# Kernel optimization log

Measured on AMD Instinct MI355X. Metric: run time of the kernel, lower is better.

## Reference

```python
import jax, jax.numpy as jnp
import numpy as np

TLAMBDA = 0.5
DELTA = 0.1
PROP_LAYERS = 2
LN_EPS = 1e-12
MASK_NEG = -10000.0
N_HEADS = 4


def _ln(x, g, b):
    m = x.mean(-1, keepdims=True)
    v = ((x - m) ** 2).mean(-1, keepdims=True)
    return (x - m) * jax.lax.rsqrt(v + LN_EPS) * g + b


def _l2norm(x):
    # F.normalize(p=2, dim=-1) with eps=1e-12
    n = jnp.sqrt((x * x).sum(-1, keepdims=True))
    return x / jnp.maximum(n, 1e-12)


def _sparse_prop(op):
    # op: [B, N, 2] rows of (col_idx, weight). result[b,j,m] = w_j*w_m if idx_j==idx_m else 0
    idx = op[..., 0].astype(jnp.int32)
    w = op[..., 1]
    eq = idx[:, :, None] == idx[:, None, :]
    return jnp.where(eq, w[:, :, None] * w[:, None, :], jnp.zeros((), op.dtype))


def _prop(t, P):
    enc = t
    for _ in range(PROP_LAYERS):
        t = jnp.einsum('bnm,bme->bne', P, t) + DELTA * enc
    return t


def _bert_layer(h, mask, Wq, bq, Wk, bk, Wv, bv, Wo, bo, g1, b1, Wi, bi, Wf, bf, g2, b2):
    AN, S, E = h.shape
    dh = E // N_HEADS

    def heads(x):
        return x.reshape(AN, S, N_HEADS, dh).transpose(0, 2, 1, 3)

    q = heads(h @ Wq + bq)
    k = heads(h @ Wk + bk)
    v = heads(h @ Wv + bv)
    scores = jnp.einsum('ahsd,ahtd->ahst', q, k) / np.float32(np.sqrt(dh)) + mask
    probs = jax.nn.softmax(scores, axis=-1)
    ctx = jnp.einsum('ahst,ahtd->ahsd', probs, v).transpose(0, 2, 1, 3).reshape(AN, S, E)
    a = _ln(ctx @ Wo + bo + h, g1, b1)
    f = jax.nn.gelu(a @ Wi + bi, approximate=False)
    return _ln(f @ Wf + bf + a, g2, b2)


def reference(token_edges_batch, hidden_states, attention_mask, query_embedding, key_embedding,
              user_operator, item_operator, distance_embedding, centrality_embedding,
              Wq, bq, Wk, bk, Wv, bv, Wo, bo, ln_att_g, ln_att_b, Wi, bi, Wf, bf, ln_ffn_g, ln_ffn_b,
              W_agg, b_agg, W_d1, b_d1, ln1_g, ln1_b, W_d2, b_d2, ln2_g, ln2_b):
    B, N, _ = token_edges_batch.shape
    AN, S, E = hidden_states.shape
    L = Wq.shape[0]

    U = _sparse_prop(user_operator)   # [B, N, N]
    I = _sparse_prop(item_operator)
    sub_next_q = jnp.zeros((B, N, E), hidden_states.dtype)
    sub_next_k = jnp.zeros((B, N, E), hidden_states.dtype)
    mask0 = attention_mask.at[..., :4].set(MASK_NEG)

    hs = hidden_states.reshape(B, N, S, E)
    all_hs = []
    for i in range(L):
        all_hs.append(hs)
        if i > 0:
            hs = (hs.at[:, :, 0].set(query_embedding)
                    .at[:, :, 1].set(key_embedding)
                    .at[:, :, 2].set(distance_embedding)
                    .at[:, :, 3].set(centrality_embedding))
        p1 = _ln(_prop(TLAMBDA * query_embedding + sub_next_q, U) @ W_d1 + b_d1, ln1_g, ln1_b)
        p2 = _ln(_prop(TLAMBDA * key_embedding + sub_next_k, I) @ W_d2 + b_d2, ln2_g, ln2_b)
        mask = mask0 if i == 0 else attention_mask
        h = _bert_layer(hs.reshape(AN, S, E), mask,
                        Wq[i], bq[i], Wk[i], bk[i], Wv[i], bv[i], Wo[i], bo[i],
                        ln_att_g[i], ln_att_b[i], Wi[i], bi[i], Wf[i], bf[i], ln_ffn_g[i], ln_ffn_b[i])
        hs = h.reshape(B, N, S, E)
        sub_next_q = hs[:, :, 0, :]
        sub_next_k = hs[:, :, 1, :]
        snt = _l2norm(hs[:, 0, 4, :])                       # [B, E]
        p = jnp.concatenate([snt, p1[:, 0, :], p2[:, 1, :]], axis=1)  # [B, 3E]
        agg = _l2norm(jax.nn.relu(p @ W_agg[i] + b_agg[i]))
        hs = hs.at[:, 0, 4, :].set(agg)
    all_hs.append(hs)

    out1 = all_hs[L - 1][:, 0, 4:, :].mean(axis=1)
    out2 = all_hs[L][:, 0, 4:, :].mean(axis=1)
    return 0.5 * (out1 + out2)


def setup_inputs() -> dict:
    key = jax.random.key(0)
    ks = jax.random.split(key, 40)
    B, N, S, E, L, FF = 64, 64, 32, 256, 2, 1024
    AN = B * N
    f = jnp.float32
    inp = {}
    inp['token_edges_batch'] = jax.random.randint(ks[0], (B, N, 8), 0, 100)
    inp['hidden_states'] = jax.random.normal(ks[1], (AN, S, E), f)
    inp['attention_mask'] = jnp.zeros((AN, 1, 1, S), f)
    inp['query_embedding'] = jax.random.normal(ks[2], (B, N, E), f)
    inp['key_embedding'] = jax.random.normal(ks[3], (B, N, E), f)
    inp['distance_embedding'] = jax.random.normal(ks[4], (B, N, E), f)
    inp['centrality_embedding'] = jax.random.normal(ks[5], (B, N, E), f)

    def make_op(k1, k2):
        idx = jax.random.randint(k1, (B, N), 0, 16).astype(f)
        w = jax.random.uniform(k2, (B, N), f)
        return jnp.stack([idx, w], axis=-1)

    inp['user_operator'] = make_op(ks[6], ks[7])
    inp['item_operator'] = make_op(ks[8], ks[9])

    sc = 0.02
    def w(k, shape):
        return jax.random.normal(k, shape, f) * sc

    inp['Wq'] = w(ks[10], (L, E, E)); inp['bq'] = jnp.zeros((L, E), f)
    inp['Wk'] = w(ks[11], (L, E, E)); inp['bk'] = jnp.zeros((L, E), f)
    inp['Wv'] = w(ks[12], (L, E, E)); inp['bv'] = jnp.zeros((L, E), f)
    inp['Wo'] = w(ks[13], (L, E, E)); inp['bo'] = jnp.zeros((L, E), f)
    inp['ln_att_g'] = jnp.ones((L, E), f); inp['ln_att_b'] = jnp.zeros((L, E), f)
    inp['Wi'] = w(ks[14], (L, E, FF)); inp['bi'] = jnp.zeros((L, FF), f)
    inp['Wf'] = w(ks[15], (L, FF, E)); inp['bf'] = jnp.zeros((L, E), f)
    inp['ln_ffn_g'] = jnp.ones((L, E), f); inp['ln_ffn_b'] = jnp.zeros((L, E), f)
    inp['W_agg'] = w(ks[16], (L, 3 * E, E)); inp['b_agg'] = jnp.zeros((L, E), f)
    inp['W_d1'] = w(ks[17], (E, E)); inp['b_d1'] = jnp.zeros((E,), f)
    inp['ln1_g'] = jnp.ones((E,), f); inp['ln1_b'] = jnp.zeros((E,), f)
    inp['W_d2'] = w(ks[18], (E, E)); inp['b_d2'] = jnp.zeros((E,), f)
    inp['ln2_g'] = jnp.ones((E,), f); inp['ln2_b'] = jnp.zeros((E,), f)
    return inp
```

## Files before the change

kernel.cpp:

```cpp
#include <hip/hip_runtime.h>
#include <math.h>

#define E 256
#define SEQ 32
#define FF 1024
#define NEG_MASK -10000.0f

typedef __attribute__((ext_vector_type(8))) short bf16x8;
typedef __attribute__((ext_vector_type(4))) short s16x4;
typedef __attribute__((ext_vector_type(4))) float f32x4;
typedef __attribute__((ext_vector_type(16))) float f32x16;

__device__ __forceinline__ float bf2f(unsigned short u) {
  unsigned v = ((unsigned)u) << 16; float f; __builtin_memcpy(&f, &v, 4); return f;
}
__device__ __forceinline__ unsigned short f2bf(float f) {
  unsigned u; __builtin_memcpy(&u, &f, 4);
  unsigned r = (u + 0x7fffu + ((u >> 16) & 1u)) >> 16;
  return (unsigned short)r;
}
__device__ __forceinline__ s16x4 f2bf4(float4 v) {
  s16x4 r;
  r[0] = (short)f2bf(v.x); r[1] = (short)f2bf(v.y);
  r[2] = (short)f2bf(v.z); r[3] = (short)f2bf(v.w);
  return r;
}
__device__ __forceinline__ f32x4 mfma16(bf16x8 a, bf16x8 b, f32x4 c) {
  return __builtin_amdgcn_mfma_f32_16x16x32_bf16(a, b, c, 0, 0, 0);
}
__device__ __forceinline__ f32x16 mfma32(bf16x8 a, bf16x8 b, f32x16 c) {
  return __builtin_amdgcn_mfma_f32_32x32x16_bf16(a, b, c, 0, 0, 0);
}
__device__ __forceinline__ float block_sum256(float v, float* tmp4) {
  #pragma unroll
  for (int o = 32; o > 0; o >>= 1) v += __shfl_down(v, o);
  int wid = threadIdx.x >> 6, lane = threadIdx.x & 63;
  if (lane == 0) tmp4[wid] = v;
  __syncthreads();
  float r = tmp4[0] + tmp4[1] + tmp4[2] + tmp4[3];
  __syncthreads();
  return r;
}

__global__ __launch_bounds__(256) void wprep_kernel(
    const float* __restrict__ Wq, const float* __restrict__ Wk,
    const float* __restrict__ Wv, const float* __restrict__ Wo,
    const float* __restrict__ Wi, const float* __restrict__ Wf,
    unsigned short* wqt, unsigned short* wkt, unsigned short* wvt,
    unsigned short* wot, unsigned short* wit, unsigned short* wft) {
  int type = blockIdx.y, ll = blockIdx.z, t = threadIdx.x;
  const float* src; unsigned short* dst; int Kd, Nd, m32;
  switch (type) {
    case 0: src = Wq + (size_t)ll * 65536;  dst = wqt + (size_t)ll * 65536;  Kd = 256;  Nd = 256;  m32 = 0; break;
    case 1: src = Wk + (size_t)ll * 65536;  dst = wkt + (size_t)ll * 65536;  Kd = 256;  Nd = 256;  m32 = 0; break;
    case 2: src = Wv + (size_t)ll * 65536;  dst = wvt + (size_t)ll * 65536;  Kd = 256;  Nd = 256;  m32 = 0; break;
    case 3: src = Wo + (size_t)ll * 65536;  dst = wot + (size_t)ll * 65536;  Kd = 256;  Nd = 256;  m32 = 0; break;
    case 4: src = Wi + (size_t)ll * 262144; dst = wit + (size_t)ll * 262144; Kd = 256;  Nd = 1024; m32 = 1; break;
    default: src = Wf + (size_t)ll * 262144; dst = wft + (size_t)ll * 262144; Kd = 1024; Nd = 256; m32 = 1; break;
  }
  int frag = blockIdx.x * 4 + (t >> 6);
  int l = t & 63;
  int nkc = m32 ? (Kd >> 4) : (Kd >> 5);
  int nfrag = (m32 ? (Nd >> 5) : (Nd >> 4)) * nkc;
  if (frag >= nfrag) return;
  int n, k0;
  if (m32) { n = (frag / nkc) * 32 + (l & 31); k0 = (frag % nkc) * 16 + (l >> 5) * 8; }
  else     { n = (frag / nkc) * 16 + (l & 15); k0 = (frag % nkc) * 32 + (l >> 4) * 8; }
  unsigned short vv[8];
  #pragma unroll
  for (int j = 0; j < 8; ++j) vv[j] = f2bf(src[(size_t)(k0 + j) * Nd + n]);
  unsigned short* o = dst + (size_t)frag * 512 + l * 8;
  #pragma unroll
  for (int j = 0; j < 8; ++j) o[j] = vv[j];
}

__global__ __launch_bounds__(256) void prop_ln_kernel(
    const float* __restrict__ emb_q, const float* __restrict__ emb_k,
    const float* snq,
    const float* __restrict__ uop, const float* __restrict__ iop,
    const float* __restrict__ Wd1, const float* __restrict__ bd1,
    const float* __restrict__ g1v, const float* __restrict__ b1v,
    const float* __restrict__ Wd2, const float* __restrict__ bd2,
    const float* __restrict__ g2v, const float* __restrict__ b2v,
    float* __restrict__ out1, float* __restrict__ out2) {
  int sel = blockIdx.y;
  const float* emb = sel ? emb_k : emb_q;
  const float* op  = sel ? iop : uop;
  const float* Wd  = sel ? Wd2 : Wd1;
  const float* bd  = sel ? bd2 : bd1;
  const float* g   = sel ? g2v : g1v;
  const float* bvec= sel ? b2v : b1v;
  float* outp      = sel ? out2 : out1;
  int row = sel;
  __shared__ float t0s[64][E];
  __shared__ float s1[16 * E];
  __shared__ float s2[16 * E];
  __shared__ float wv[64];
  __shared__ int gi[64];
  __shared__ float t2row[E];
  __shared__ float tmp4[4];
  int b = blockIdx.x, e = threadIdx.x;
  if (e < 64) {
    wv[e] = op[(b * 64 + e) * 2 + 1];
    gi[e] = (int)op[(b * 64 + e) * 2 + 0];
  }
  for (int gg = 0; gg < 16; ++gg) { s1[gg * E + e] = 0.f; s2[gg * E + e] = 0.f; }
  for (int n = 0; n < 64; ++n) {
    float t0 = 0.5f * emb[(size_t)(b * 64 + n) * E + e];
    if (snq) t0 += snq[((size_t)(b * 64 + n) * 2 + sel) * E + e];
    t0s[n][e] = t0;
  }
  __syncthreads();
  for (int n = 0; n < 64; ++n) s1[gi[n] * E + e] += wv[n] * t0s[n][e];
  for (int n = 0; n < 64; ++n) {
    float t1 = wv[n] * s1[gi[n] * E + e] + 0.1f * t0s[n][e];
    s2[gi[n] * E + e] += wv[n] * t1;
  }
  float t2 = wv[row] * s2[gi[row] * E + e] + 0.1f * t0s[row][e];
  t2row[e] = t2;
  __syncthreads();
  float y = bd[e];
  for (int k = 0; k < E; ++k) y = fmaf(t2row[k], Wd[k * E + e], y);
  float ssum = block_sum256(y, tmp4);
  float qsum = block_sum256(y * y, tmp4);
  float m = ssum * (1.f / E);
  float var = qsum * (1.f / E) - m * m;
  outp[b * E + e] = (y - m) * rsqrtf(var + 1e-12f) * g[e] + bvec[e];
}

__global__ __launch_bounds__(256, 4) void seq_attn_mfma(
    const float* __restrict__ hidden,
    const unsigned short* __restrict__ wqt, const float* __restrict__ bq,
    const unsigned short* __restrict__ wkt, const float* __restrict__ bk,
    const unsigned short* __restrict__ wvt, const float* __restrict__ bv,
    const float* __restrict__ mask, unsigned short* __restrict__ ctx_all,
    unsigned short* __restrict__ Kf, unsigned short* __restrict__ Vf) {
  __shared__ __align__(16) unsigned short aT[32][264];
  __shared__ __align__(16) unsigned short kvb[32][272];
  __shared__ __align__(16) unsigned short qs16[2][264];
  __shared__ float pr[4][2][36];
  int a = blockIdx.x, t = threadIdx.x;
  int w = t >> 6, l = t & 63;
  int lm = l & 15, lkq = l >> 4, lk = lkq << 3;
  size_t hb = (size_t)a * (SEQ * E);
  #pragma unroll
  for (int i = 0; i < 8; ++i) {
    int p = i * 256 + t; int row = p >> 6, c4 = (p & 63) << 2;
    float4 v = *(const float4*)&hidden[hb + row * E + c4];
    *(s16x4*)&aT[row][c4] = f2bf4(v);
  }
  __syncthreads();
  bool isn0 = ((a & 63) == 0);
  int nb = a >> 6;
  f32x4 zz = {0.f, 0.f, 0.f, 0.f};
  #pragma unroll
  for (int nt = 0; nt < 4; ++nt) {
    int ncol = w * 64 + nt * 16 + lm;
    const unsigned short* bkrow = wkt + ((size_t)(w * 4 + nt) * 8) * 512 + l * 8;
    const unsigned short* bqrow = wqt + ((size_t)(w * 4 + nt) * 8) * 512 + l * 8;
    bf16x8 bk8[8], bq8[8];
    #pragma unroll
    for (int kc = 0; kc < 8; ++kc) bk8[kc] = *(const bf16x8*)(bkrow + kc * 512);
    #pragma unroll
    for (int kc = 0; kc < 8; ++kc) bq8[kc] = *(const bf16x8*)(bqrow + kc * 512);
    f32x4 ak0 = zz, ak1 = zz, aq = zz;
    #pragma unroll
    for (int kc = 0; kc < 8; ++kc) {
      bf16x8 a0 = *(const bf16x8*)&aT[lm][kc * 32 + lk];
      bf16x8 a1 = *(const bf16x8*)&aT[16 + lm][kc * 32 + lk];
      ak0 = mfma16(a0, bk8[kc], ak0);
      ak1 = mfma16(a1, bk8[kc], ak1);
      aq  = mfma16(a0, bq8[kc], aq);
    }
    float bb = bk[ncol];
    #pragma unroll
    for (int r = 0; r < 4; ++r) {
      int rw = (lkq << 2) + r;
      float v0 = ak0[r] + bb, v1 = ak1[r] + bb;
      kvb[rw][ncol] = f2bf(v0);
      kvb[16 + rw][ncol] = f2bf(v1);
      if (isn0) {
        Kf[((size_t)nb * 32 + rw) * 256 + ncol] = f2bf(v0);
        Kf[((size_t)nb * 32 + 16 + rw) * 256 + ncol] = f2bf(v1);
      }
    }
    if (lkq == 0) {
      float bqv = bq[ncol];
      qs16[0][ncol] = f2bf(aq[0] + bqv);
      qs16[1][ncol] = f2bf(aq[1] + bqv);
    }
  }
  __syncthreads();
  {
    f32x4 sc0 = zz, sc1 = zz;
    #pragma unroll
    for (int kc2 = 0; kc2 < 2; ++kc2) {
      bf16x8 aq = *(const bf16x8*)&qs16[lm & 1][w * 64 + kc2 * 32 + lk];
      bf16x8 b0 = *(const bf16x8*)&kvb[lm][w * 64 + kc2 * 32 + lk];
      bf16x8 b1 = *(const bf16x8*)&kvb[16 + lm][w * 64 + kc2 * 32 + lk];
      sc0 = mfma16(aq, b0, sc0);
      sc1 = mfma16(aq, b1, sc1);
    }
    float mv0 = (lm < 4) ? NEG_MASK : mask[(size_t)a * SEQ + lm];
    float mv1 = mask[(size_t)a * SEQ + 16 + lm];
    #pragma unroll
    for (int r = 0; r < 2; ++r) {
      float s0 = sc0[r] * 0.125f + mv0;
      float s1 = sc1[r] * 0.125f + mv1;
      float mx = fmaxf(s0, s1);
      mx = fmaxf(mx, __shfl_xor(mx, 1));
      mx = fmaxf(mx, __shfl_xor(mx, 2));
      mx = fmaxf(mx, __shfl_xor(mx, 4));
      mx = fmaxf(mx, __shfl_xor(mx, 8));
      float e0 = expf(s0 - mx), e1 = expf(s1 - mx);
      float se = e0 + e1;
      se += __shfl_xor(se, 1); se += __shfl_xor(se, 2);
      se += __shfl_xor(se, 4); se += __shfl_xor(se, 8);
      float inv = 1.f / se;
      if (lkq == 0) {
        pr[w][r][lm] = e0 * inv;
        pr[w][r][16 + lm] = e1 * inv;
      }
    }
  }
  __syncthreads();
  #pragma unroll
  for (int nt = 0; nt < 4; ++nt) {
    int ncol = w * 64 + nt * 16 + lm;
    const unsigned short* bvrow = wvt + ((size_t)(w * 4 + nt) * 8) * 512 + l * 8;
    bf16x8 bv8[8];
    #pragma unroll
    for (int kc = 0; kc < 8; ++kc) bv8[kc] = *(const bf16x8*)(bvrow + kc * 512);
    f32x4 av0 = zz, av1 = zz;
    #pragma unroll
    for (int kc = 0; kc < 8; ++kc) {
      bf16x8 a0 = *(const bf16x8*)&aT[lm][kc * 32 + lk];
      bf16x8 a1 = *(const bf16x8*)&aT[16 + lm][kc * 32 + lk];
      av0 = mfma16(a0, bv8[kc], av0);
      av1 = mfma16(a1, bv8[kc], av1);
    }
    float bb = bv[ncol];
    #pragma unroll
    for (int r = 0; r < 4; ++r) {
      int rw = (lkq << 2) + r;
      float v0 = av0[r] + bb, v1 = av1[r] + bb;
      kvb[rw][ncol] = f2bf(v0);
      kvb[16 + rw][ncol] = f2bf(v1);
      if (isn0) {
        Vf[((size_t)nb * 32 + rw) * 256 + ncol] = f2bf(v0);
        Vf[((size_t)nb * 32 + 16 + rw) * 256 + ncol] = f2bf(v1);
      }
    }
  }
  __syncthreads();
  {
    float o0 = 0.f, o1 = 0.f;
    #pragma unroll
    for (int tt = 0; tt < 32; ++tt) {
      float vv = bf2f(kvb[tt][t]);
      o0 = fmaf(pr[w][0][tt], vv, o0);
      o1 = fmaf(pr[w][1][tt], vv, o1);
    }
    ctx_all[((size_t)a * 2 + 0) * E + t] = f2bf(o0);
    ctx_all[((size_t)a * 2 + 1) * E + t] = f2bf(o1);
  }
}

__global__ __launch_bounds__(256) void gemm_bias_kernel(
    const float* __restrict__ Af, const unsigned short* __restrict__ Bt,
    const float* __restrict__ bias, unsigned short* __restrict__ outb) {
  __shared__ __align__(16) unsigned short aT[32][264];
  int t = threadIdx.x, w = t >> 6, l = t & 63;
  int lm = l & 15, lkq = l >> 4, lk = lkq << 3;
  int row0 = blockIdx.x * 32;
  #pragma unroll
  for (int i = 0; i < 8; ++i) {
    int p = i * 256 + t; int row = p >> 6, c4 = (p & 63) << 2;
    int gr = row0 + row;
    int src = ((gr >> 5) << 11) + (gr & 31);
    float4 v = *(const float4*)&Af[(size_t)src * E + c4];
    *(s16x4*)&aT[row][c4] = f2bf4(v);
  }
  __syncthreads();
  f32x4 zz = {0.f, 0.f, 0.f, 0.f};
  #pragma unroll
  for (int nt = 0; nt < 4; ++nt) {
    int ncol = w * 64 + nt * 16 + lm;
    const unsigned short* brow = Bt + ((size_t)(w * 4 + nt) * 8) * 512 + l * 8;
    bf16x8 b8[8];
    #pragma unroll
    for (int kc = 0; kc < 8; ++kc) b8[kc] = *(const bf16x8*)(brow + kc * 512);
    f32x4 c0 = zz, c1 = zz;
    #pragma unroll
    for (int kc = 0; kc < 8; ++kc) {
      bf16x8 a0 = *(const bf16x8*)&aT[lm][kc * 32 + lk];
      bf16x8 a1 = *(const bf16x8*)&aT[16 + lm][kc * 32 + lk];
      c0 = mfma16(a0, b8[kc], c0);
      c1 = mfma16(a1, b8[kc], c1);
    }
    float bb = bias[ncol];
    #pragma unroll
    for (int r = 0; r < 4; ++r) {
      int rw = (lkq << 2) + r;
      outb[(size_t)(row0 + rw) * E + ncol] = f2bf(c0[r] + bb);
      outb[(size_t)(row0 + 16 + rw) * E + ncol] = f2bf(c1[r] + bb);
    }
  }
}

__global__ __launch_bounds__(256) void qkv1_kernel(
    const unsigned short* __restrict__ Ab,
    const unsigned short* __restrict__ wq, const float* __restrict__ bqv,
    const unsigned short* __restrict__ wk, const float* __restrict__ bkv,
    const unsigned short* __restrict__ wv, const float* __restrict__ bvv,
    unsigned short* q2, unsigned short* k2, unsigned short* v2) {
  __shared__ __align__(16) unsigned short aT[32][264];
  int t = threadIdx.x, w = t >> 6, l = t & 63;
  int lm = l & 15, lkq = l >> 4, lk = lkq << 3;
  int row0 = blockIdx.x * 32;
  int m = blockIdx.y;
  const unsigned short* Wt = (m == 0) ? wq : (m == 1) ? wk : wv;
  const float* bb = (m == 0) ? bqv : (m == 1) ? bkv : bvv;
  unsigned short* outb = (m == 0) ? q2 : (m == 1) ? k2 : v2;
  #pragma unroll
  for (int i = 0; i < 4; ++i) {
    int p = i * 256 + t; int row = p >> 5, c8 = (p & 31) << 3;
    *(s16x4*)&aT[row][c8] = *(const s16x4*)&Ab[(size_t)(row0 + row) * E + c8];
    *(s16x4*)&aT[row][c8 + 4] = *(const s16x4*)&Ab[(size_t)(row0 + row) * E + c8 + 4];
  }
  __syncthreads();
  f32x4 zz = {0.f, 0.f, 0.f, 0.f};
  #pragma unroll
  for (int nt = 0; nt < 4; ++nt) {
    int ncol = w * 64 + nt * 16 + lm;
    const unsigned short* brow = Wt + ((size_t)(w * 4 + nt) * 8) * 512 + l * 8;
    bf16x8 b8[8];
    #pragma unroll
    for (int kc = 0; kc < 8; ++kc) b8[kc] = *(const bf16x8*)(brow + kc * 512);
    f32x4 c0 = zz, c1 = zz;
    #pragma unroll
    for (int kc = 0; kc < 8; ++kc) {
      bf16x8 a0 = *(const bf16x8*)&aT[lm][kc * 32 + lk];
      bf16x8 a1 = *(const bf16x8*)&aT[16 + lm][kc * 32 + lk];
      c0 = mfma16(a0, b8[kc], c0);
      c1 = mfma16(a1, b8[kc], c1);
    }
    float bv2 = bb[ncol];
    #pragma unroll
    for (int r = 0; r < 4; ++r) {
      int rw = (lkq << 2) + r;
      outb[(size_t)(row0 + rw) * E + ncol] = f2bf(c0[r] + bv2);
      outb[(size_t)(row0 + 16 + rw) * E + ncol] = f2bf(c1[r] + bv2);
    }
  }
}

__global__ __launch_bounds__(256) void attnf_kernel(
    const unsigned short* __restrict__ Q, const unsigned short* __restrict__ K,
    const unsigned short* __restrict__ V, unsigned short* __restrict__ CTX,
    const float* __restrict__ mask, int set4) {
  int b = blockIdx.x, h = blockIdx.y, t = threadIdx.x;
  __shared__ float qsh[32][65], ksh[32][65], vsh[32][65];
  __shared__ float pr[32][33];
  size_t base = (size_t)b * (SEQ * E) + h * 64;
  for (int i = 0; i < 8; ++i) {
    int p = i * 256 + t; int s = p >> 6, d = p & 63;
    qsh[s][d] = bf2f(Q[base + s * E + d]);
    ksh[s][d] = bf2f(K[base + s * E + d]);
    vsh[s][d] = bf2f(V[base + s * E + d]);
  }
  __syncthreads();
  for (int i = 0; i < 4; ++i) {
    int p = i * 256 + t; int s = p >> 5, tt = p & 31;
    float acc = 0.f;
    #pragma unroll
    for (int d = 0; d < 64; ++d) acc = fmaf(qsh[s][d], ksh[tt][d], acc);
    float mv = mask[(size_t)b * 2048 + tt];
    if (set4 && tt < 4) mv = NEG_MASK;
    pr[s][tt] = acc * 0.125f + mv;
  }
  __syncthreads();
  int rrow = t >> 3, l8 = t & 7;
  float vals[4];
  float mx = -1e30f;
  #pragma unroll
  for (int ii = 0; ii < 4; ++ii) { vals[ii] = pr[rrow][l8 + ii * 8]; mx = fmaxf(mx, vals[ii]); }
  mx = fmaxf(mx, __shfl_xor(mx, 1));
  mx = fmaxf(mx, __shfl_xor(mx, 2));
  mx = fmaxf(mx, __shfl_xor(mx, 4));
  float se = 0.f;
  #pragma unroll
  for (int ii = 0; ii < 4; ++ii) { vals[ii] = expf(vals[ii] - mx); se += vals[ii]; }
  se += __shfl_xor(se, 1); se += __shfl_xor(se, 2); se += __shfl_xor(se, 4);
  float inv = 1.f / se;
  #pragma unroll
  for (int ii = 0; ii < 4; ++ii) pr[rrow][l8 + ii * 8] = vals[ii] * inv;
  __syncthreads();
  for (int i = 0; i < 8; ++i) {
    int p = i * 256 + t; int s = p >> 6, d = p & 63;
    float acc = 0.f;
    #pragma unroll
    for (int tt = 0; tt < SEQ; ++tt) acc = fmaf(pr[s][tt], vsh[tt][d], acc);
    CTX[base + s * E + d] = f2bf(acc);
  }
}

__device__ __forceinline__ int map_res(int gr) {
  if (gr < 8192) return ((gr >> 1) << 5) + (gr & 1);
  int rr = gr - 8192;
  return ((rr >> 5) << 11) + (rr & 31);
}

__global__ __launch_bounds__(256) void tailA_mfma(
    const unsigned short* __restrict__ ctx,
    const unsigned short* __restrict__ wo, const float* __restrict__ bo,
    const float* __restrict__ Res, int resmode,
    const float* __restrict__ g1, const float* __restrict__ b1,
    unsigned short* __restrict__ a_bf, float* __restrict__ a_f32) {
  __shared__ __align__(16) unsigned short aT[32][264];
  __shared__ float sT[32][257];
  __shared__ float prs[32][4], prq[32][4];
  int t = threadIdx.x, w = t >> 6, l = t & 63;
  int row0 = blockIdx.x * 32;
  #pragma unroll
  for (int i = 0; i < 8; ++i) {
    int p = i * 256 + t; int row = p >> 6, c4 = (p & 63) << 2;
    *(s16x4*)&aT[row][c4] = *(const s16x4*)&ctx[(size_t)(row0 + row) * E + c4];
  }
  __syncthreads();
  {
    int lm = l & 15, lkq = l >> 4, lk = lkq << 3;
    f32x4 zz = {0.f, 0.f, 0.f, 0.f};
    #pragma unroll
    for (int nt = 0; nt < 4; ++nt) {
      int ncol = w * 64 + nt * 16 + lm;
      const unsigned short* brow = wo + ((size_t)(w * 4 + nt) * 8) * 512 + l * 8;
      bf16x8 b8[8];
      #pragma unroll
      for (int kc = 0; kc < 8; ++kc) b8[kc] = *(const bf16x8*)(brow + kc * 512);
      f32x4 c0 = zz, c1 = zz;
      #pragma unroll
      for (int kc = 0; kc < 8; ++kc) {
        bf16x8 a0 = *(const bf16x8*)&aT[lm][kc * 32 + lk];
        bf16x8 a1 = *(const bf16x8*)&aT[16 + lm][kc * 32 + lk];
        c0 = mfma16(a0, b8[kc], c0);
        c1 = mfma16(a1, b8[kc], c1);
      }
      float bb = bo[ncol];
      #pragma unroll
      for (int r = 0; r < 4; ++r) {
        int rw = (lkq << 2) + r;
        int rr0 = resmode ? map_res(row0 + rw) : (row0 + rw);
        int rr1 = resmode ? map_res(row0 + 16 + rw) : (row0 + 16 + rw);
        sT[rw][ncol] = c0[r] + bb + Res[(size_t)rr0 * E + ncol];
        sT[16 + rw][ncol] = c1[r] + bb + Res[(size_t)rr1 * E + ncol];
      }
    }
  }
  __syncthreads();
  {
    int wid = t >> 6, lane = t & 63;
    float vcache[32];
    for (int r = 0; r < 32; ++r) {
      float v = sT[r][t];
      vcache[r] = v;
      float s = v, q = v * v;
      #pragma unroll
      for (int o = 32; o > 0; o >>= 1) { s += __shfl_down(s, o); q += __shfl_down(q, o); }
      if (lane == 0) { prs[r][wid] = s; prq[r][wid] = q; }
    }
    __syncthreads();
    #pragma unroll
    for (int r = 0; r < 32; ++r) {
      float Sv = prs[r][0] + prs[r][1] + prs[r][2] + prs[r][3];
      float Qv = prq[r][0] + prq[r][1] + prq[r][2] + prq[r][3];
      float m = Sv * (1.f / E), var = Qv * (1.f / E) - m * m;
      float val = (vcache[r] - m) * rsqrtf(var + 1e-12f) * g1[t] + b1[t];
      a_f32[(size_t)(row0 + r) * E + t] = val;
      a_bf[(size_t)(row0 + r) * E + t] = f2bf(val);
    }
  }
}

__global__ __launch_bounds__(512) void ffnB_kernel(
    const unsigned short* __restrict__ a_bf,
    const unsigned short* __restrict__ wi, const float* __restrict__ bi,
    const unsigned short* __restrict__ wf,
    float* __restrict__ part, size_t pstride) {
  __shared__ __align__(16) unsigned short aT[32][264];
  __shared__ __align__(16) unsigned short fT[32][264];
  int t = threadIdx.x, w = t >> 6, l = t & 63;
  int lm = l & 31, lk = (l >> 5) << 3;
  int row0 = blockIdx.x * 32, qh = blockIdx.y;
  #pragma unroll
  for (int i = 0; i < 2; ++i) {
    int chunk = i * 512 + t; int row = chunk >> 5, c8 = (chunk & 31) << 3;
    *(s16x4*)&aT[row][c8] = *(const s16x4*)&a_bf[(size_t)(row0 + row) * E + c8];
    *(s16x4*)&aT[row][c8 + 4] = *(const s16x4*)&a_bf[(size_t)(row0 + row) * E + c8 + 4];
  }
  __syncthreads();
  f32x16 zz16 = {0};
  {
    const unsigned short* brow = wi + ((size_t)(qh * 8 + w) * 16) * 512 + l * 8;
    bf16x8 b16[16];
    #pragma unroll
    for (int kc = 0; kc < 16; ++kc) b16[kc] = *(const bf16x8*)(brow + kc * 512);
    f32x16 c = zz16;
    #pragma unroll
    for (int kc = 0; kc < 16; ++kc) {
      bf16x8 a = *(const bf16x8*)&aT[lm][kc * 16 + lk];
      c = mfma32(a, b16[kc], c);
    }
    int lcol = w * 32 + lm;
    float bib = bi[qh * 256 + lcol];
    #pragma unroll
    for (int reg = 0; reg < 16; ++reg) {
      int row = (reg & 3) + 8 * (reg >> 2) + 4 * (l >> 5);
      float x = c[reg] + bib;
      fT[row][lcol] = f2bf(0.5f * x * (1.f + erff(x * 0.70710678118654752f)));
    }
  }
  __syncthreads();
  {
    const unsigned short* brow = wf + ((size_t)(w * 64 + qh * 16)) * 512 + l * 8;
    bf16x8 b16[16];
    #pragma unroll
    for (int kc = 0; kc < 16; ++kc) b16[kc] = *(const bf16x8*)(brow + kc * 512);
    f32x16 c = zz16;
    #pragma unroll
    for (int kc = 0; kc < 16; ++kc) {
      bf16x8 a = *(const bf16x8*)&fT[lm][kc * 16 + lk];
      c = mfma32(a, b16[kc], c);
    }
    float* po = part + (size_t)qh * pstride;
    int col = w * 32 + lm;
    #pragma unroll
    for (int reg = 0; reg < 16; ++reg) {
      int row = (reg & 3) + 8 * (reg >> 2) + 4 * (l >> 5);
      po[(size_t)(row0 + row) * E + col] = c[reg];
    }
  }
}

__global__ __launch_bounds__(256) void ffnC_kernel(
    const float* __restrict__ part, size_t pstride,
    const float* __restrict__ bfv, const float* __restrict__ a_f32,
    const float* __restrict__ g2, const float* __restrict__ b2,
    float* __restrict__ out0, float* __restrict__ out1, int split) {
  __shared__ float prs[32][4], prq[32][4];
  int t = threadIdx.x;
  int row0 = blockIdx.x * 32;
  int wid = t >> 6, lane = t & 63;
  float bb = bfv[t];
  float vcache[32];
  for (int r = 0; r < 32; ++r) {
    size_t idx = (size_t)(row0 + r) * E + t;
    float v = part[idx] + part[pstride + idx] + part[2 * pstride + idx] +
              part[3 * pstride + idx] + bb + a_f32[idx];
    vcache[r] = v;
    float s = v, q = v * v;
    #pragma unroll
    for (int o = 32; o > 0; o >>= 1) { s += __shfl_down(s, o); q += __shfl_down(q, o); }
    if (lane == 0) { prs[r][wid] = s; prq[r][wid] = q; }
  }
  __syncthreads();
  #pragma unroll
  for (int r = 0; r < 32; ++r) {
    float Sv = prs[r][0] + prs[r][1] + prs[r][2] + prs[r][3];
    float Qv = prq[r][0] + prq[r][1] + prq[r][2] + prq[r][3];
    float m = Sv * (1.f / E), var = Qv * (1.f / E) - m * m;
    float val = (vcache[r] - m) * rsqrtf(var + 1e-12f) * g2[t] + b2[t];
    int gr = row0 + r;
    if (gr < split) out0[(size_t)gr * E + t] = val;
    else            out1[(size_t)(gr - split) * E + t] = val;
  }
}

__global__ __launch_bounds__(256) void agg_build_kernel(
    const float* __restrict__ h1n0,
    const float* __restrict__ p1, const float* __restrict__ p2,
    const float* __restrict__ Wagg, const float* __restrict__ bagg,
    const float* __restrict__ qe, const float* __restrict__ ke,
    const float* __restrict__ de, const float* __restrict__ ce,
    float* __restrict__ agg0,
    float* __restrict__ h2f, unsigned short* __restrict__ h2b) {
  __shared__ float pv[768];
  __shared__ float tmp4[4];
  int b = blockIdx.x, t = threadIdx.x;
  float x = h1n0[(size_t)b * (SEQ * E) + 4 * E + t];
  float n2 = block_sum256(x * x, tmp4);
  pv[t] = x / fmaxf(sqrtf(n2), 1e-12f);
  pv[256 + t] = p1[b * E + t];
  pv[512 + t] = p2[b * E + t];
  __syncthreads();
  float y = bagg[t];
  for (int u = 0; u < 768; ++u) y = fmaf(pv[u], Wagg[u * E + t], y);
  y = fmaxf(y, 0.f);
  float n3 = block_sum256(y * y, tmp4);
  float aggv = y / fmaxf(sqrtf(n3), 1e-12f);
  agg0[b * E + t] = aggv;
  size_t eb = (size_t)(b * 64) * E + t;
  size_t ob = (size_t)b * (SEQ * E);
  float v;
  v = qe[eb];  h2f[ob + 0 * E + t] = v; h2b[ob + 0 * E + t] = f2bf(v);
  v = ke[eb];  h2f[ob + 1 * E + t] = v; h2b[ob + 1 * E + t] = f2bf(v);
  v = de[eb];  h2f[ob + 2 * E + t] = v; h2b[ob + 2 * E + t] = f2bf(v);
  v = ce[eb];  h2f[ob + 3 * E + t] = v; h2b[ob + 3 * E + t] = f2bf(v);
  h2f[ob + 4 * E + t] = aggv; h2b[ob + 4 * E + t] = f2bf(aggv);
  for (int s = 5; s < SEQ; ++s) {
    v = h1n0[ob + s * E + t];
    h2f[ob + s * E + t] = v; h2b[ob + s * E + t] = f2bf(v);
  }
}

__global__ __launch_bounds__(256) void agg_kernel(
    const float* __restrict__ hbase,
    const float* __restrict__ p1, const float* __restrict__ p2,
    const float* __restrict__ Wagg, const float* __restrict__ bagg,
    float* __restrict__ outp) {
  __shared__ float pv[768];
  __shared__ float tmp4[4];
  int b = blockIdx.x, t = threadIdx.x;
  float x = hbase[(size_t)b * (SEQ * E) + 4 * E + t];
  float n2 = block_sum256(x * x, tmp4);
  pv[t] = x / fmaxf(sqrtf(n2), 1e-12f);
  pv[256 + t] = p1[b * E + t];
  pv[512 + t] = p2[b * E + t];
  __syncthreads();
  float y = bagg[t];
  for (int u = 0; u < 768; ++u) y = fmaf(pv[u], Wagg[u * E + t], y);
  y = fmaxf(y, 0.f);
  float n3 = block_sum256(y * y, tmp4);
  outp[b * E + t] = y / fmaxf(sqrtf(n3), 1e-12f);
}

__global__ __launch_bounds__(256) void out_kernel(
    const float* __restrict__ h1n0, const float* __restrict__ agg0,
    const float* __restrict__ h2, const float* __restrict__ agg1,
    float* __restrict__ outp) {
  int b = blockIdx.x, t = threadIdx.x;
  size_t ob = (size_t)b * (SEQ * E);
  float s1v = agg0[b * E + t];
  float s2v = agg1[b * E + t];
  for (int s = 5; s < SEQ; ++s) { s1v += h1n0[ob + s * E + t]; s2v += h2[ob + s * E + t]; }
  outp[b * E + t] = 0.5f * (s1v + s2v) * (1.f / 28.f);
}

extern "C" void kernel_launch(void* const* d_in, const int* in_sizes, int n_in,
                              void* d_out, int out_size, void* d_ws, size_t ws_size,
                              hipStream_t stream) {
  (void)in_sizes; (void)n_in; (void)out_size;
  const float* hidden = (const float*)d_in[1];
  const float* amask  = (const float*)d_in[2];
  const float* qemb   = (const float*)d_in[3];
  const float* kemb   = (const float*)d_in[4];
  const float* demb   = (const float*)d_in[5];
  const float* cemb   = (const float*)d_in[6];
  const float* uop    = (const float*)d_in[7];
  const float* iop    = (const float*)d_in[8];
  const float* Wq = (const float*)d_in[9];  const float* bq = (const float*)d_in[10];
  const float* Wk = (const float*)d_in[11]; const float* bk = (const float*)d_in[12];
  const float* Wv = (const float*)d_in[13]; const float* bv = (const float*)d_in[14];
  const float* Wo = (const float*)d_in[15]; const float* bo = (const float*)d_in[16];
  const float* g1 = (const float*)d_in[17]; const float* b1 = (const float*)d_in[18];
  const float* Wi = (const float*)d_in[19]; const float* bi = (const float*)d_in[20];
  const float* Wf = (const float*)d_in[21]; const float* bf = (const float*)d_in[22];
  const float* g2 = (const float*)d_in[23]; const float* b2 = (const float*)d_in[24];
  const float* Wagg = (const float*)d_in[25]; const float* bagg = (const float*)d_in[26];
  const float* Wd1 = (const float*)d_in[27]; const float* bd1 = (const float*)d_in[28];
  const float* l1g = (const float*)d_in[29]; const float* l1b = (const float*)d_in[30];
  const float* Wd2 = (const float*)d_in[31]; const float* bd2 = (const float*)d_in[32];
  const float* l2g = (const float*)d_in[33]; const float* l2b = (const float*)d_in[34];

  char* cur = (char*)d_ws;
  auto alloc_us = [&](size_t n) { unsigned short* p = (unsigned short*)cur; cur += ((n * 2 + 255) & ~(size_t)255); return p; };
  auto alloc_f  = [&](size_t n) { float* p = (float*)cur; cur += ((n * 4 + 255) & ~(size_t)255); return p; };
  unsigned short* wqt = alloc_us(131072);
  unsigned short* wkt = alloc_us(131072);
  unsigned short* wvt = alloc_us(131072);
  unsigned short* wot = alloc_us(131072);
  unsigned short* wit = alloc_us(524288);
  unsigned short* wft = alloc_us(524288);
  unsigned short* ctx_all = alloc_us((size_t)10240 * 256);
  unsigned short* qn0 = alloc_us((size_t)2048 * 256);
  unsigned short* Kf  = alloc_us((size_t)2048 * 256);
  unsigned short* Vf  = alloc_us((size_t)2048 * 256);
  unsigned short* h2inb = alloc_us((size_t)2048 * 256);
  unsigned short* a_bf = alloc_us((size_t)10240 * 256);
  unsigned short* q2b = alloc_us((size_t)2048 * 256);
  unsigned short* k2b = alloc_us((size_t)2048 * 256);
  unsigned short* v2b = alloc_us((size_t)2048 * 256);
  unsigned short* ctx1 = alloc_us((size_t)2048 * 256);
  float* a_f32 = alloc_f((size_t)10240 * 256);
  float* part  = alloc_f((size_t)4 * 10240 * 256);
  float* h101  = alloc_f((size_t)4096 * 2 * 256);
  float* h1n0  = alloc_f((size_t)2048 * 256);
  float* h2inf = alloc_f((size_t)2048 * 256);
  float* h2    = alloc_f((size_t)2048 * 256);
  float* p1_0  = alloc_f(64 * 256);
  float* p2_0  = alloc_f(64 * 256);
  float* p1_1  = alloc_f(64 * 256);
  float* p2_1  = alloc_f(64 * 256);
  float* agg0  = alloc_f(64 * 256);
  float* agg1  = alloc_f(64 * 256);
  if ((size_t)(cur - (char*)d_ws) > ws_size) return;
  const size_t PSTRIDE = (size_t)10240 * 256;

  wprep_kernel<<<dim3(128, 6, 2), 256, 0, stream>>>(Wq, Wk, Wv, Wo, Wi, Wf,
                                                    wqt, wkt, wvt, wot, wit, wft);

  prop_ln_kernel<<<dim3(64, 2), 256, 0, stream>>>(qemb, kemb, nullptr, uop, iop,
                                                  Wd1, bd1, l1g, l1b, Wd2, bd2, l2g, l2b,
                                                  p1_0, p2_0);
  seq_attn_mfma<<<4096, 256, 0, stream>>>(hidden, wqt, bq, wkt, bk, wvt, bv,
                                          amask, ctx_all, Kf, Vf);
  gemm_bias_kernel<<<64, 256, 0, stream>>>(hidden, wqt, bq, qn0);
  attnf_kernel<<<dim3(64, 4), 256, 0, stream>>>(qn0, Kf, Vf, ctx_all + (size_t)8192 * 256,
                                                amask, 1);
  tailA_mfma<<<320, 256, 0, stream>>>(ctx_all, wot, bo, hidden, 1, g1, b1, a_bf, a_f32);
  ffnB_kernel<<<dim3(320, 4), 512, 0, stream>>>(a_bf, wit, bi, wft, part, PSTRIDE);
  ffnC_kernel<<<320, 256, 0, stream>>>(part, PSTRIDE, bf, a_f32, g2, b2,
                                       h101, h1n0, 8192);
  agg_build_kernel<<<64, 256, 0, stream>>>(h1n0, p1_0, p2_0, Wagg, bagg,
                                           qemb, kemb, demb, cemb, agg0, h2inf, h2inb);

  prop_ln_kernel<<<dim3(64, 2), 256, 0, stream>>>(qemb, kemb, h101, uop, iop,
                                                  Wd1, bd1, l1g, l1b, Wd2, bd2, l2g, l2b,
                                                  p1_1, p2_1);
  qkv1_kernel<<<dim3(64, 3), 256, 0, stream>>>(h2inb,
                                               wqt + 65536, bq + E,
                                               wkt + 65536, bk + E,
                                               wvt + 65536, bv + E,
                                               q2b, k2b, v2b);
  attnf_kernel<<<dim3(64, 4), 256, 0, stream>>>(q2b, k2b, v2b, ctx1, amask, 0);
  tailA_mfma<<<64, 256, 0, stream>>>(ctx1, wot + 65536, bo + E, h2inf, 0,
                                     g1 + E, b1 + E, a_bf, a_f32);
  ffnB_kernel<<<dim3(64, 4), 512, 0, stream>>>(a_bf, wit + 262144, bi + FF,
                                               wft + 262144, part, PSTRIDE);
  ffnC_kernel<<<64, 256, 0, stream>>>(part, PSTRIDE, bf + E, a_f32,
                                      g2 + E, b2 + E, h2, h2, 1 << 30);
  agg_kernel<<<64, 256, 0, stream>>>(h2, p1_1, p2_1,
                                     Wagg + (size_t)768 * E, bagg + E, agg1);

  out_kernel<<<64, 256, 0, stream>>>(h1n0, agg0, h2, agg1, (float*)d_out);
}
```

Before: 386.7 us.

## Fuse V projection into QK loop, fold Q GEMM and agg/out kernels

The V projection now runs inside the same loop as the K/Q MFMAs and its results are kept in registers, so the A-tile is read from LDS once instead of twice. The standalone gemm_bias kernel is removed: the n==0 blocks of seq_attn compute the full Q rows and write qn0 directly. agg_kernel and out_kernel are merged into one launch, and prop_ln drops its 64x256 shared t0 buffer by recomputing t0 from global memory. This saves two launches and some LDS traffic, but costs more registers (avreg, extra bv8 loads) under launch_bounds(256,4), which can cause spills or lower occupancy.

```diff
diff --git a/kernel.cpp b/kernel.cpp
--- a/kernel.cpp
+++ b/kernel.cpp
@@ -92,7 +92,6 @@
   const float* bvec= sel ? b2v : b1v;
   float* outp      = sel ? out2 : out1;
   int row = sel;
-  __shared__ float t0s[64][E];
   __shared__ float s1[16 * E];
   __shared__ float s2[16 * E];
   __shared__ float wv[64];
@@ -105,18 +104,21 @@
     gi[e] = (int)op[(b * 64 + e) * 2 + 0];
   }
   for (int gg = 0; gg < 16; ++gg) { s1[gg * E + e] = 0.f; s2[gg * E + e] = 0.f; }
+  __syncthreads();
+  float t0r = 0.f;
   for (int n = 0; n < 64; ++n) {
     float t0 = 0.5f * emb[(size_t)(b * 64 + n) * E + e];
     if (snq) t0 += snq[((size_t)(b * 64 + n) * 2 + sel) * E + e];
-    t0s[n][e] = t0;
-  }
-  __syncthreads();
-  for (int n = 0; n < 64; ++n) s1[gi[n] * E + e] += wv[n] * t0s[n][e];
+    if (n == row) t0r = t0;
+    s1[gi[n] * E + e] += wv[n] * t0;
+  }
   for (int n = 0; n < 64; ++n) {
-    float t1 = wv[n] * s1[gi[n] * E + e] + 0.1f * t0s[n][e];
+    float t0 = 0.5f * emb[(size_t)(b * 64 + n) * E + e];
+    if (snq) t0 += snq[((size_t)(b * 64 + n) * 2 + sel) * E + e];
+    float t1 = wv[n] * s1[gi[n] * E + e] + 0.1f * t0;
     s2[gi[n] * E + e] += wv[n] * t1;
   }
-  float t2 = wv[row] * s2[gi[row] * E + e] + 0.1f * t0s[row][e];
+  float t2 = wv[row] * s2[gi[row] * E + e] + 0.1f * t0r;
   t2row[e] = t2;
   __syncthreads();
   float y = bd[e];
@@ -134,6 +136,7 @@
     const unsigned short* __restrict__ wkt, const float* __restrict__ bk,
     const unsigned short* __restrict__ wvt, const float* __restrict__ bv,
     const float* __restrict__ mask, unsigned short* __restrict__ ctx_all,
+    unsigned short* __restrict__ qn0,
     unsigned short* __restrict__ Kf, unsigned short* __restrict__ Vf) {
   __shared__ __align__(16) unsigned short aT[32][264];
   __shared__ __align__(16) unsigned short kvb[32][272];
@@ -153,30 +156,36 @@
   bool isn0 = ((a & 63) == 0);
   int nb = a >> 6;
   f32x4 zz = {0.f, 0.f, 0.f, 0.f};
+  f32x4 avreg[4][2];
   #pragma unroll
   for (int nt = 0; nt < 4; ++nt) {
     int ncol = w * 64 + nt * 16 + lm;
     const unsigned short* bkrow = wkt + ((size_t)(w * 4 + nt) * 8) * 512 + l * 8;
     const unsigned short* bqrow = wqt + ((size_t)(w * 4 + nt) * 8) * 512 + l * 8;
-    bf16x8 bk8[8], bq8[8];
+    const unsigned short* bvrow = wvt + ((size_t)(w * 4 + nt) * 8) * 512 + l * 8;
+    bf16x8 bk8[8], bq8[8], bv8[8];
     #pragma unroll
     for (int kc = 0; kc < 8; ++kc) bk8[kc] = *(const bf16x8*)(bkrow + kc * 512);
     #pragma unroll
     for (int kc = 0; kc < 8; ++kc) bq8[kc] = *(const bf16x8*)(bqrow + kc * 512);
-    f32x4 ak0 = zz, ak1 = zz, aq = zz;
+    #pragma unroll
+    for (int kc = 0; kc < 8; ++kc) bv8[kc] = *(const bf16x8*)(bvrow + kc * 512);
+    f32x4 ak0 = zz, ak1 = zz, aq = zz, av0 = zz, av1 = zz;
     #pragma unroll
     for (int kc = 0; kc < 8; ++kc) {
-      bf16x8 a0 = *(const bf16x8*)&aT[lm][kc * 32 + lk];
-      bf16x8 a1 = *(const bf16x8*)&aT[16 + lm][kc * 32 + lk];
-      ak0 = mfma16(a0, bk8[kc], ak0);
-      ak1 = mfma16(a1, bk8[kc], ak1);
-      aq  = mfma16(a0, bq8[kc], aq);
-    }
-    float bb = bk[ncol];
+      bf16x8 a0f = *(const bf16x8*)&aT[lm][kc * 32 + lk];
+      bf16x8 a1f = *(const bf16x8*)&aT[16 + lm][kc * 32 + lk];
+      ak0 = mfma16(a0f, bk8[kc], ak0);
+      ak1 = mfma16(a1f, bk8[kc], ak1);
+      aq  = mfma16(a0f, bq8[kc], aq);
+      av0 = mfma16(a0f, bv8[kc], av0);
+      av1 = mfma16(a1f, bv8[kc], av1);
+    }
+    float bbk = bk[ncol];
     #pragma unroll
     for (int r = 0; r < 4; ++r) {
       int rw = (lkq << 2) + r;
-      float v0 = ak0[r] + bb, v1 = ak1[r] + bb;
+      float v0 = ak0[r] + bbk, v1 = ak1[r] + bbk;
       kvb[rw][ncol] = f2bf(v0);
       kvb[16 + rw][ncol] = f2bf(v1);
       if (isn0) {
@@ -188,6 +197,33 @@
       float bqv = bq[ncol];
       qs16[0][ncol] = f2bf(aq[0] + bqv);
       qs16[1][ncol] = f2bf(aq[1] + bqv);
+    }
+    avreg[nt][0] = av0;
+    avreg[nt][1] = av1;
+  }
+  if (isn0) {
+    #pragma unroll
+    for (int nt = 0; nt < 4; ++nt) {
+      int ncol = w * 64 + nt * 16 + lm;
+      const unsigned short* bqrow = wqt + ((size_t)(w * 4 + nt) * 8) * 512 + l * 8;
+      bf16x8 bq8[8];
+      #pragma unroll
+      for (int kc = 0; kc < 8; ++kc) bq8[kc] = *(const bf16x8*)(bqrow + kc * 512);
+      f32x4 q0 = zz, q1 = zz;
+      #pragma unroll
+      for (int kc = 0; kc < 8; ++kc) {
+        bf16x8 a0f = *(const bf16x8*)&aT[lm][kc * 32 + lk];
+        bf16x8 a1f = *(const bf16x8*)&aT[16 + lm][kc * 32 + lk];
+        q0 = mfma16(a0f, bq8[kc], q0);
+        q1 = mfma16(a1f, bq8[kc], q1);
+      }
+      float bqv = bq[ncol];
+      #pragma unroll
+      for (int r = 0; r < 4; ++r) {
+        int rw = (lkq << 2) + r;
+        qn0[((size_t)nb * 32 + rw) * 256 + ncol] = f2bf(q0[r] + bqv);
+        qn0[((size_t)nb * 32 + 16 + rw) * 256 + ncol] = f2bf(q1[r] + bqv);
+      }
     }
   }
   __syncthreads();
@@ -227,23 +263,11 @@
   #pragma unroll
   for (int nt = 0; nt < 4; ++nt) {
     int ncol = w * 64 + nt * 16 + lm;
-    const unsigned short* bvrow = wvt + ((size_t)(w * 4 + nt) * 8) * 512 + l * 8;
-    bf16x8 bv8[8];
-    #pragma unroll
-    for (int kc = 0; kc < 8; ++kc) bv8[kc] = *(const bf16x8*)(bvrow + kc * 512);
-    f32x4 av0 = zz, av1 = zz;
-    #pragma unroll
-    for (int kc = 0; kc < 8; ++kc) {
-      bf16x8 a0 = *(const bf16x8*)&aT[lm][kc * 32 + lk];
-      bf16x8 a1 = *(const bf16x8*)&aT[16 + lm][kc * 32 + lk];
-      av0 = mfma16(a0, bv8[kc], av0);
-      av1 = mfma16(a1, bv8[kc], av1);
-    }
-    float bb = bv[ncol];
+    float bbv = bv[ncol];
     #pragma unroll
     for (int r = 0; r < 4; ++r) {
       int rw = (lkq << 2) + r;
-      float v0 = av0[r] + bb, v1 = av1[r] + bb;
+      float v0 = avreg[nt][0][r] + bbv, v1 = avreg[nt][1][r] + bbv;
       kvb[rw][ncol] = f2bf(v0);
       kvb[16 + rw][ncol] = f2bf(v1);
       if (isn0) {
@@ -263,48 +287,6 @@
     }
     ctx_all[((size_t)a * 2 + 0) * E + t] = f2bf(o0);
     ctx_all[((size_t)a * 2 + 1) * E + t] = f2bf(o1);
-  }
-}
-
-__global__ __launch_bounds__(256) void gemm_bias_kernel(
-    const float* __restrict__ Af, const unsigned short* __restrict__ Bt,
-    const float* __restrict__ bias, unsigned short* __restrict__ outb) {
-  __shared__ __align__(16) unsigned short aT[32][264];
-  int t = threadIdx.x, w = t >> 6, l = t & 63;
-  int lm = l & 15, lkq = l >> 4, lk = lkq << 3;
-  int row0 = blockIdx.x * 32;
-  #pragma unroll
-  for (int i = 0; i < 8; ++i) {
-    int p = i * 256 + t; int row = p >> 6, c4 = (p & 63) << 2;
-    int gr = row0 + row;
-    int src = ((gr >> 5) << 11) + (gr & 31);
-    float4 v = *(const float4*)&Af[(size_t)src * E + c4];
-    *(s16x4*)&aT[row][c4] = f2bf4(v);
-  }
-  __syncthreads();
-  f32x4 zz = {0.f, 0.f, 0.f, 0.f};
-  #pragma unroll
-  for (int nt = 0; nt < 4; ++nt) {
-    int ncol = w * 64 + nt * 16 + lm;
-    const unsigned short* brow = Bt + ((size_t)(w * 4 + nt) * 8) * 512 + l * 8;
-    bf16x8 b8[8];
-    #pragma unroll
-    for (int kc = 0; kc < 8; ++kc) b8[kc] = *(const bf16x8*)(brow + kc * 512);
-    f32x4 c0 = zz, c1 = zz;
-    #pragma unroll
-    for (int kc = 0; kc < 8; ++kc) {
-      bf16x8 a0 = *(const bf16x8*)&aT[lm][kc * 32 + lk];
-      bf16x8 a1 = *(const bf16x8*)&aT[16 + lm][kc * 32 + lk];
-      c0 = mfma16(a0, b8[kc], c0);
-      c1 = mfma16(a1, b8[kc], c1);
-    }
-    float bb = bias[ncol];
-    #pragma unroll
-    for (int r = 0; r < 4; ++r) {
-      int rw = (lkq << 2) + r;
-      outb[(size_t)(row0 + rw) * E + ncol] = f2bf(c0[r] + bb);
-      outb[(size_t)(row0 + 16 + rw) * E + ncol] = f2bf(c1[r] + bb);
-    }
   }
 }
 
@@ -613,15 +595,16 @@
   }
 }
 
-__global__ __launch_bounds__(256) void agg_kernel(
-    const float* __restrict__ hbase,
+__global__ __launch_bounds__(256) void agg_out_kernel(
+    const float* __restrict__ h2,
     const float* __restrict__ p1, const float* __restrict__ p2,
     const float* __restrict__ Wagg, const float* __restrict__ bagg,
+    const float* __restrict__ h1n0, const float* __restrict__ agg0,
     float* __restrict__ outp) {
   __shared__ float pv[768];
   __shared__ float tmp4[4];
   int b = blockIdx.x, t = threadIdx.x;
-  float x = hbase[(size_t)b * (SEQ * E) + 4 * E + t];
+  float x = h2[(size_t)b * (SEQ * E) + 4 * E + t];
   float n2 = block_sum256(x * x, tmp4);
   pv[t] = x / fmaxf(sqrtf(n2), 1e-12f);
   pv[256 + t] = p1[b * E + t];
@@ -631,17 +614,10 @@
   for (int u = 0; u < 768; ++u) y = fmaf(pv[u], Wagg[u * E + t], y);
   y = fmaxf(y, 0.f);
   float n3 = block_sum256(y * y, tmp4);
-  outp[b * E + t] = y / fmaxf(sqrtf(n3), 1e-12f);
-}
-
-__global__ __launch_bounds__(256) void out_kernel(
-    const float* __restrict__ h1n0, const float* __restrict__ agg0,
-    const float* __restrict__ h2, const float* __restrict__ agg1,
-    float* __restrict__ outp) {
-  int b = blockIdx.x, t = threadIdx.x;
+  float agg1v = y / fmaxf(sqrtf(n3), 1e-12f);
   size_t ob = (size_t)b * (SEQ * E);
   float s1v = agg0[b * E + t];
-  float s2v = agg1[b * E + t];
+  float s2v = agg1v;
   for (int s = 5; s < SEQ; ++s) { s1v += h1n0[ob + s * E + t]; s2v += h2[ob + s * E + t]; }
   outp[b * E + t] = 0.5f * (s1v + s2v) * (1.f / 28.f);
 }
@@ -702,7 +678,6 @@
   float* p1_1  = alloc_f(64 * 256);
   float* p2_1  = alloc_f(64 * 256);
   float* agg0  = alloc_f(64 * 256);
-  float* agg1  = alloc_f(64 * 256);
   if ((size_t)(cur - (char*)d_ws) > ws_size) return;
   const size_t PSTRIDE = (size_t)10240 * 256;
 
@@ -713,8 +688,7 @@
                                                   Wd1, bd1, l1g, l1b, Wd2, bd2, l2g, l2b,
                                                   p1_0, p2_0);
   seq_attn_mfma<<<4096, 256, 0, stream>>>(hidden, wqt, bq, wkt, bk, wvt, bv,
-                                          amask, ctx_all, Kf, Vf);
-  gemm_bias_kernel<<<64, 256, 0, stream>>>(hidden, wqt, bq, qn0);
+                                          amask, ctx_all, qn0, Kf, Vf);
   attnf_kernel<<<dim3(64, 4), 256, 0, stream>>>(qn0, Kf, Vf, ctx_all + (size_t)8192 * 256,
                                                 amask, 1);
   tailA_mfma<<<320, 256, 0, stream>>>(ctx_all, wot, bo, hidden, 1, g1, b1, a_bf, a_f32);
@@ -739,8 +713,7 @@
                                                wft + 262144, part, PSTRIDE);
   ffnC_kernel<<<64, 256, 0, stream>>>(part, PSTRIDE, bf + E, a_f32,
                                       g2 + E, b2 + E, h2, h2, 1 << 30);
-  agg_kernel<<<64, 256, 0, stream>>>(h2, p1_1, p2_1,
-                                     Wagg + (size_t)768 * E, bagg + E, agg1);
-
-  out_kernel<<<64, 256, 0, stream>>>(h1n0, agg0, h2, agg1, (float*)d_out);
-}
+  agg_out_kernel<<<64, 256, 0, stream>>>(h2, p1_1, p2_1,
+                                         Wagg + (size_t)768 * E, bagg + E,
+                                         h1n0, agg0, (float*)d_out);
+}
```

Measured after the change: 588.6 us. 52.2% more time.
